# Kernel tuning notes

Measured on AMD Instinct MI355X. Metric: run time of the kernel, lower is better.

The kernel has to match this reference:

```python
import jax, jax.numpy as jnp
import numpy as np

D = 768       # GATv2 in/out feats (num_heads=1)
D_OUT = 384   # fc output
K = 51        # round(top_rate * L) = round(0.1 * 512)
EPS = 1e-5    # nn.LayerNorm default eps


def _layer_norm(x, g, b):
    mu = jnp.mean(x, axis=-1, keepdims=True)
    var = jnp.mean((x - mu) ** 2, axis=-1, keepdims=True)
    return (x - mu) / jnp.sqrt(var + EPS) * g + b


def setup_inputs() -> dict:
    key = jax.random.key(0)
    ks = jax.random.split(key, 12)
    B, L = 4, 512
    s = 0.02
    return {
        "hidden_state": jax.random.normal(ks[0], (B, L, D), jnp.float32),
        "attention": jax.random.uniform(ks[1], (B, L, L), jnp.float32),
        # GATv2Conv params (fc_src, fc_dst, attn vector, output bias)
        "W_src": jax.random.normal(ks[2], (D, D), jnp.float32) * s,
        "b_src": jnp.zeros((D,), jnp.float32),
        "W_dst": jax.random.normal(ks[3], (D, D), jnp.float32) * s,
        "b_dst": jnp.zeros((D,), jnp.float32),
        "attn_vec": jax.random.normal(ks[4], (D,), jnp.float32) * s,
        "gat_bias": jnp.zeros((D,), jnp.float32),
        # GlobalAttentionPooling gate_nn: Linear(768, 1)
        "gate_W": jax.random.normal(ks[5], (D, 1), jnp.float32) * s,
        "gate_b": jnp.zeros((1,), jnp.float32),
        # LayerNorm(768)
        "ln_g": jnp.ones((D,), jnp.float32),
        "ln_b": jnp.zeros((D,), jnp.float32),
        # fc: Linear(768, 384)
        "fc_W": jax.random.normal(ks[6], (D, D_OUT), jnp.float32) * s,
        "fc_b": jnp.zeros((D_OUT,), jnp.float32),
        # LayerNorm(384)
        "ln2_g": jnp.ones((D_OUT,), jnp.float32),
        "ln2_b": jnp.zeros((D_OUT,), jnp.float32),
        "mask": jnp.ones((B, L), jnp.int32),  # unused by the original forward
        "type": 0,                              # unused string/type flag
    }


def reference(hidden_state, attention, W_src, b_src, W_dst, b_dst, attn_vec,
              gat_bias, gate_W, gate_b, ln_g, ln_b, fc_W, fc_b, ln2_g, ln2_b,
              mask, type):
    B, L, _ = hidden_state.shape
    # --- topk sparsification: each node i keeps K source neighbors ---
    vals, idx = jax.lax.top_k(attention, K)          # [B, L, K]
    valid = vals > 0.0                                # edges kept by pos_sign filter

    # --- GATv2Conv (num_heads=1, residual=Identity since 768==768) ---
    feat_src = hidden_state @ W_src + b_src           # [B, L, D]
    feat_dst = hidden_state @ W_dst + b_dst           # [B, L, D]
    g = feat_src[jnp.arange(B)[:, None, None], idx]   # [B, L, K, D] gathered src feats
    e = jax.nn.leaky_relu(g + feat_dst[:, :, None, :], 0.2)
    scores = jnp.einsum("blkd,d->blk", e, attn_vec)   # [B, L, K]
    scores = jnp.where(valid, scores, -1e9)           # removed edges masked out
    a = jax.nn.softmax(scores, axis=-1)               # edge_softmax per dst node
    h = jnp.einsum("blk,blkd->bld", a, g)             # weighted scatter-sum
    h = h + hidden_state + gat_bias                   # residual (identity) + bias
    h = jax.nn.leaky_relu(h, 0.01)                    # nn.LeakyReLU activation

    # --- GlobalAttentionPooling: softmax(gate) weighted segment reduce ---
    gate = h @ gate_W + gate_b                        # [B, L, 1]
    p = jax.nn.softmax(gate, axis=1)
    pooled = jnp.sum(p * h, axis=1)                   # [B, D]

    # --- head: fc(dropout(ln(relu(out)))) then ln2 (dropout = eval identity) ---
    out = _layer_norm(jax.nn.relu(pooled), ln_g, ln_b)
    out = out @ fc_W + fc_b
    out = _layer_norm(out, ln2_g, ln2_b)
    return out
```

## Files before the change

kernel.cpp:

```cpp
#include <hip/hip_runtime.h>
#include <math.h>

#define D 768
#define DOUT 384
#define LSEQ 512
#define BATCH 4
#define KTOP 51
#define EPS 1e-5f

typedef unsigned short ushort_t;
typedef __bf16 bf16x8 __attribute__((ext_vector_type(8)));
typedef float f32x4 __attribute__((ext_vector_type(4)));

#define GLOAD16(gp, lp)                                                        \
    __builtin_amdgcn_global_load_lds(                                          \
        (const __attribute__((address_space(1))) unsigned int*)(gp),           \
        (__attribute__((address_space(3))) unsigned int*)(lp), 16, 0, 0)

__device__ __forceinline__ ushort_t f2bf(float f) {
    unsigned int u = __builtin_bit_cast(unsigned int, f);
    u = (u + 0x7FFFu + ((u >> 16) & 1u)) >> 16;
    return (ushort_t)u;
}

__global__ __launch_bounds__(256) void prep_kernel(const float* __restrict__ hidden,
                                                   ushort_t* __restrict__ Ah,
                                                   const float* __restrict__ W0,
                                                   const float* __restrict__ W1,
                                                   ushort_t* __restrict__ WT0,
                                                   ushort_t* __restrict__ WT1) {
    __shared__ float tile[32][33];
    const int bid = blockIdx.x;
    const int tid = threadIdx.x;
    if (bid < 1536) {
        const int i = (bid * 256 + tid) * 4;
        const float4 v = *(const float4*)(hidden + i);
        ushort4 o;
        o.x = f2bf(v.x); o.y = f2bf(v.y); o.z = f2bf(v.z); o.w = f2bf(v.w);
        *(ushort4*)(Ah + i) = o;
    } else {
        const int t = bid - 1536;
        const int zz = t / 576;
        const int rem = t - zz * 576;
        const int by = rem / 24, bx = rem - by * 24;
        const float* W = zz ? W1 : W0;
        ushort_t* WT = zz ? WT1 : WT0;
        const int kbase = by * 32;
        const int nbase = bx * 32;
        const int r = tid >> 3, c4 = (tid & 7) * 4;

        const float4 v = *(const float4*)(W + (size_t)(kbase + r) * D + nbase + c4);
        tile[r][c4 + 0] = v.x; tile[r][c4 + 1] = v.y;
        tile[r][c4 + 2] = v.z; tile[r][c4 + 3] = v.w;
        __syncthreads();
        ushort4 o;
        o.x = f2bf(tile[c4 + 0][r]); o.y = f2bf(tile[c4 + 1][r]);
        o.z = f2bf(tile[c4 + 2][r]); o.w = f2bf(tile[c4 + 3][r]);
        *(ushort4*)(WT + (size_t)(nbase + r) * D + kbase + c4) = o;
    }
}

__global__ __launch_bounds__(256) void feat_gemm_kernel(const ushort_t* __restrict__ Ah,
                                                        const ushort_t* __restrict__ WT0,
                                                        const float* __restrict__ b0,
                                                        ushort_t* __restrict__ Csrc_bf,
                                                        const ushort_t* __restrict__ WT1,
                                                        const float* __restrict__ b1,
                                                        float* __restrict__ Cdst) {
    const ushort_t* WT = blockIdx.z ? WT1 : WT0;
    const float* bias = blockIdx.z ? b1 : b0;

    __shared__ ushort_t As[64 * 32];
    __shared__ ushort_t Bs[64 * 32];

    const int tid = threadIdx.x;
    const int lane = tid & 63;
    const int wave = tid >> 6;
    const int quad = lane >> 4;
    const int m15 = lane & 15;
    const int qRow = (wave & 1) * 32;
    const int qCol = (wave >> 1) * 32;

    const int rowBase = blockIdx.y * 64;
    const int colBase = blockIdx.x * 64;

    const int e0 = tid * 8;
    const int r0 = e0 >> 5;
    const int c0 = e0 & 31;
    const ushort_t* Abase = Ah + (size_t)rowBase * D;
    const ushort_t* Bbase = WT + (size_t)colBase * D;

    f32x4 acc[2][2] = {};

    for (int kk = 0; kk < D; kk += 32) {
        __syncthreads();
        GLOAD16(Abase + (size_t)r0 * D + kk + c0, &As[e0]);
        GLOAD16(Bbase + (size_t)r0 * D + kk + c0, &Bs[e0]);
        __syncthreads();

        bf16x8 a[2], b[2];
#pragma unroll
        for (int i = 0; i < 2; ++i)
            a[i] = *(const bf16x8*)&As[(qRow + i * 16 + m15) * 32 + quad * 8];
#pragma unroll
        for (int j = 0; j < 2; ++j)
            b[j] = *(const bf16x8*)&Bs[(qCol + j * 16 + m15) * 32 + quad * 8];
#pragma unroll
        for (int i = 0; i < 2; ++i)
#pragma unroll
            for (int j = 0; j < 2; ++j)
                acc[i][j] = __builtin_amdgcn_mfma_f32_16x16x32_bf16(a[i], b[j], acc[i][j], 0, 0, 0);
    }

    if (blockIdx.z == 0) {
#pragma unroll
        for (int j = 0; j < 2; ++j) {
            const int col = colBase + qCol + j * 16 + m15;
            const float bv = bias[col];
#pragma unroll
            for (int i = 0; i < 2; ++i) {
                ushort_t* Cp = Csrc_bf + (size_t)(rowBase + qRow + i * 16 + quad * 4) * D + col;
#pragma unroll
                for (int r = 0; r < 4; ++r)
                    Cp[(size_t)r * D] = f2bf(acc[i][j][r] + bv);
            }
        }
    } else {
#pragma unroll
        for (int j = 0; j < 2; ++j) {
            const int col = colBase + qCol + j * 16 + m15;
            const float bv = bias[col];
#pragma unroll
            for (int i = 0; i < 2; ++i) {
                float* Cp = Cdst + (size_t)(rowBase + qRow + i * 16 + quad * 4) * D + col;
#pragma unroll
                for (int r = 0; r < 4; ++r)
                    Cp[(size_t)r * D] = acc[i][j][r] + bv;
            }
        }
    }
}

__global__ __launch_bounds__(256) void transpose_fsrc_kernel(const ushort_t* __restrict__ I,
                                                             ushort_t* __restrict__ O) {
    __shared__ ushort_t tile[32][33];
    const int b = blockIdx.z;
    const int cbase = blockIdx.x * 32;
    const int rbase = blockIdx.y * 32;
    const int tid = threadIdx.x;
    const int tr = tid >> 3, tc4 = (tid & 7) * 4;

    const ushort_t* Ib = I + (size_t)b * LSEQ * D;
    ushort_t* Ob = O + (size_t)b * D * LSEQ;

    const ushort4 v = *(const ushort4*)(Ib + (size_t)(rbase + tr) * D + cbase + tc4);
    tile[tr][tc4 + 0] = v.x; tile[tr][tc4 + 1] = v.y;
    tile[tr][tc4 + 2] = v.z; tile[tr][tc4 + 3] = v.w;
    __syncthreads();
    ushort4 o;
    o.x = tile[tc4 + 0][tr]; o.y = tile[tc4 + 1][tr];
    o.z = tile[tc4 + 2][tr]; o.w = tile[tc4 + 3][tr];
    *(ushort4*)(Ob + (size_t)(cbase + tr) * LSEQ + rbase + tc4) = o;
}

__global__ __launch_bounds__(256) void score_kernel(const float* __restrict__ attn,
                                                    const ushort_t* __restrict__ fsrc_bf,
                                                    const float* __restrict__ feat_dst,
                                                    const float* __restrict__ attn_vec,
                                                    const float* __restrict__ gate_b,
                                                    ushort_t* __restrict__ P,
                                                    float* __restrict__ gate) {
    const int row = blockIdx.x;
    const int b = row >> 9;
    const int tid = threadIdx.x;
    const int lane = tid & 63;
    const int wave = tid >> 6;

    __shared__ float vals[LSEQ];
    __shared__ float cval[320];
    __shared__ int   cidx[320];
    __shared__ int   nhi, outSlot;
    __shared__ float sc[KTOP];
    __shared__ int   kid[KTOP];
    __shared__ float kvv[KTOP];

    ((unsigned int*)(P + (size_t)row * LSEQ))[tid] = 0u;
    if (tid == 0) { gate[row] = gate_b[0]; nhi = 0; outSlot = 0; }

    const float* a = attn + (size_t)row * LSEQ;
    const float v0 = a[tid];
    const float v1 = a[tid + 256];
    vals[tid] = v0;
    vals[tid + 256] = v1;
    __syncthreads();

    if (v0 > 0.75f) {
        const int s = atomicAdd(&nhi, 1);
        if (s < 320) { cval[s] = v0; cidx[s] = tid; }
    }
    if (v1 > 0.75f) {
        const int s = atomicAdd(&nhi, 1);
        if (s < 320) { cval[s] = v1; cidx[s] = tid + 256; }
    }
    __syncthreads();

    const int n = nhi;
    if (n >= KTOP && n <= 320) {
        if (tid < n) {
            const float v = cval[tid];
            const int e = cidx[tid];
            int r = 0;
            for (int j = 0; j < n; ++j) {
                const float u = cval[j];
                r += (u > v) || (u == v && cidx[j] < e);
            }
            if (r < KTOP) {
                const int s = atomicAdd(&outSlot, 1);
                kid[s] = e; kvv[s] = v;
            }
        }
    } else {
#pragma unroll
        for (int e0 = 0; e0 < 2; ++e0) {
            const int e = tid + e0 * 256;
            const float v = vals[e];
            int r = 0;
            for (int j = 0; j < LSEQ; ++j) {
                const float u = vals[j];
                r += (u > v) || (u == v && j < e);
            }
            if (r < KTOP) {
                const int s = atomicAdd(&outSlot, 1);
                kid[s] = e; kvv[s] = v;
            }
        }
    }

    const float* fdp = feat_dst + (size_t)row * D;
    float fdr[16], avr[16];
    {
        const int d0 = lane * 8;
        const float4 f0 = *(const float4*)(fdp + d0);
        const float4 f1 = *(const float4*)(fdp + d0 + 4);
        const float4 a0 = *(const float4*)(attn_vec + d0);
        const float4 a1 = *(const float4*)(attn_vec + d0 + 4);
        fdr[0]=f0.x; fdr[1]=f0.y; fdr[2]=f0.z; fdr[3]=f0.w;
        fdr[4]=f1.x; fdr[5]=f1.y; fdr[6]=f1.z; fdr[7]=f1.w;
        avr[0]=a0.x; avr[1]=a0.y; avr[2]=a0.z; avr[3]=a0.w;
        avr[4]=a1.x; avr[5]=a1.y; avr[6]=a1.z; avr[7]=a1.w;
    }
    if (lane < 32) {
        const int d1 = (lane + 64) * 8;
        const float4 f0 = *(const float4*)(fdp + d1);
        const float4 f1 = *(const float4*)(fdp + d1 + 4);
        const float4 a0 = *(const float4*)(attn_vec + d1);
        const float4 a1 = *(const float4*)(attn_vec + d1 + 4);
        fdr[8]=f0.x; fdr[9]=f0.y; fdr[10]=f0.z; fdr[11]=f0.w;
        fdr[12]=f1.x; fdr[13]=f1.y; fdr[14]=f1.z; fdr[15]=f1.w;
        avr[8]=a0.x; avr[9]=a0.y; avr[10]=a0.z; avr[11]=a0.w;
        avr[12]=a1.x; avr[13]=a1.y; avr[14]=a1.z; avr[15]=a1.w;
    }
    __syncthreads();

    for (int k = wave; k < KTOP; k += 4) {
        const ushort_t* g = fsrc_bf + ((size_t)(b << 9) + kid[k]) * D;
        float s = 0.f;
        const bf16x8 g0 = *(const bf16x8*)(g + lane * 8);
#pragma unroll
        for (int jj = 0; jj < 8; ++jj) {
            float x = (float)g0[jj] + fdr[jj];
            x = x > 0.f ? x : 0.2f * x;
            s += x * avr[jj];
        }
        if (lane < 32) {
            const bf16x8 g1 = *(const bf16x8*)(g + (lane + 64) * 8);
#pragma unroll
            for (int jj = 0; jj < 8; ++jj) {
                float x = (float)g1[jj] + fdr[8 + jj];
                x = x > 0.f ? x : 0.2f * x;
                s += x * avr[8 + jj];
            }
        }
#pragma unroll
        for (int off = 32; off > 0; off >>= 1) s += __shfl_down(s, off);
        if (lane == 0) sc[k] = (kvv[k] > 0.f) ? s : -1e9f;
    }
    __syncthreads();

    if (wave == 0) {
        float s = (lane < KTOP) ? sc[lane] : -3.0e38f;
        float m = s;
#pragma unroll
        for (int off = 32; off > 0; off >>= 1) m = fmaxf(m, __shfl_xor(m, off));
        float e = (lane < KTOP) ? __expf(s - m) : 0.f;
        float sum = e;
#pragma unroll
        for (int off = 32; off > 0; off >>= 1) sum += __shfl_xor(sum, off);
        if (lane < KTOP) sc[lane] = e / sum;
    }
    __syncthreads();

    if (tid < KTOP)
        P[(size_t)row * LSEQ + kid[tid]] = f2bf(sc[tid]);
}

__global__ __launch_bounds__(256) void pgemm_kernel(const ushort_t* __restrict__ P,
                                                    const ushort_t* __restrict__ fsrcT,
                                                    const float* __restrict__ gat_bias,
                                                    const float* __restrict__ hidden,
                                                    const float* __restrict__ gate_W,
                                                    float* __restrict__ h,
                                                    float* __restrict__ gate) {
    const int bb = blockIdx.z;
    const ushort_t* Ab = P + (size_t)bb * LSEQ * LSEQ;
    const ushort_t* Bb = fsrcT + (size_t)bb * D * LSEQ;

    __shared__ ushort_t As[64 * 32];
    __shared__ ushort_t Bs[64 * 32];

    const int tid = threadIdx.x;
    const int lane = tid & 63;
    const int wave = tid >> 6;
    const int quad = lane >> 4;
    const int m15 = lane & 15;
    const int qRow = (wave & 1) * 32;
    const int qCol = (wave >> 1) * 32;

    const int rowBase = blockIdx.y * 64;
    const int colBase = blockIdx.x * 64;

    const int e0 = tid * 8;
    const int r0 = e0 >> 5;
    const int c0 = e0 & 31;
    const ushort_t* Abase = Ab + (size_t)rowBase * LSEQ;
    const ushort_t* Bbase = Bb + (size_t)colBase * LSEQ;

    f32x4 acc[2][2] = {};

    for (int kk = 0; kk < LSEQ; kk += 32) {
        __syncthreads();
        GLOAD16(Abase + (size_t)r0 * LSEQ + kk + c0, &As[e0]);
        GLOAD16(Bbase + (size_t)r0 * LSEQ + kk + c0, &Bs[e0]);
        __syncthreads();

        bf16x8 a[2], b[2];
#pragma unroll
        for (int i = 0; i < 2; ++i)
            a[i] = *(const bf16x8*)&As[(qRow + i * 16 + m15) * 32 + quad * 8];
#pragma unroll
        for (int j = 0; j < 2; ++j)
            b[j] = *(const bf16x8*)&Bs[(qCol + j * 16 + m15) * 32 + quad * 8];
#pragma unroll
        for (int i = 0; i < 2; ++i)
#pragma unroll
            for (int j = 0; j < 2; ++j)
                acc[i][j] = __builtin_amdgcn_mfma_f32_16x16x32_bf16(a[i], b[j], acc[i][j], 0, 0, 0);
    }

    const float* hidb = hidden + (size_t)bb * LSEQ * D;
    float* hb = h + (size_t)bb * LSEQ * D;
    float rp[2][4] = {};
#pragma unroll
    for (int j = 0; j < 2; ++j) {
        const int col = colBase + qCol + j * 16 + m15;
        const float bv = gat_bias[col];
        const float gw = gate_W[col];
#pragma unroll
        for (int i = 0; i < 2; ++i) {
            const int row0 = rowBase + qRow + i * 16 + quad * 4;
#pragma unroll
            for (int r = 0; r < 4; ++r) {
                float v = acc[i][j][r] + bv + hidb[(size_t)(row0 + r) * D + col];
                v = v > 0.f ? v : 0.01f * v;
                hb[(size_t)(row0 + r) * D + col] = v;
                rp[i][r] += v * gw;
            }
        }
    }
#pragma unroll
    for (int i = 0; i < 2; ++i)
#pragma unroll
        for (int r = 0; r < 4; ++r) {
            float p4 = rp[i][r];
            p4 += __shfl_xor(p4, 1);
            p4 += __shfl_xor(p4, 2);
            p4 += __shfl_xor(p4, 4);
            p4 += __shfl_xor(p4, 8);
            if (m15 == 0)
                atomicAdd(&gate[bb * LSEQ + rowBase + qRow + i * 16 + quad * 4 + r], p4);
        }
}

__global__ __launch_bounds__(256) void gatesm_kernel(const float* __restrict__ gate,
                                                     float* __restrict__ p,
                                                     float* __restrict__ pooled,
                                                     float* __restrict__ z) {
    const int b = blockIdx.x;
    const int tid = threadIdx.x;
    __shared__ float red[256];

    const float g0 = gate[b * LSEQ + tid];
    const float g1 = gate[b * LSEQ + tid + 256];
    red[tid] = fmaxf(g0, g1);
    __syncthreads();
    for (int s = 128; s > 0; s >>= 1) { if (tid < s) red[tid] = fmaxf(red[tid], red[tid + s]); __syncthreads(); }
    const float m = red[0];
    __syncthreads();
    const float e0 = __expf(g0 - m), e1 = __expf(g1 - m);
    red[tid] = e0 + e1;
    __syncthreads();
    for (int s = 128; s > 0; s >>= 1) { if (tid < s) red[tid] += red[tid + s]; __syncthreads(); }
    const float inv = 1.f / red[0];
    p[b * LSEQ + tid] = e0 * inv;
    p[b * LSEQ + tid + 256] = e1 * inv;

    for (int d = tid; d < D; d += 256) pooled[b * D + d] = 0.f;
    if (tid < 128) { z[b * DOUT + tid] = 0.f; z[b * DOUT + tid + 128] = 0.f; z[b * DOUT + tid + 256] = 0.f; }
}

__global__ __launch_bounds__(256) void pool_kernel(const float* __restrict__ h,
                                                   const float* __restrict__ p,
                                                   float* __restrict__ pooled) {
    const int b = blockIdx.z;
    const int lbase = blockIdx.y * 64;
    const int d = blockIdx.x * 256 + threadIdx.x;
    const int tid = threadIdx.x;

    __shared__ float ps[64];
    if (tid < 64) ps[tid] = p[b * LSEQ + lbase + tid];
    __syncthreads();

    const float* hb = h + ((size_t)(b * LSEQ + lbase)) * D + d;
    float acc = 0.f;
#pragma unroll 8
    for (int l = 0; l < 64; ++l) {
        acc += ps[l] * hb[(size_t)l * D];
    }
    atomicAdd(&pooled[b * D + d], acc);
}

__global__ __launch_bounds__(256) void ln1_kernel(const float* __restrict__ pooled,
                                                  const float* __restrict__ ln_g,
                                                  const float* __restrict__ ln_b,
                                                  float* __restrict__ y) {
    const int b = blockIdx.x;
    const int tid = threadIdx.x;
    __shared__ float red[256];

    float v[3];
#pragma unroll
    for (int i = 0; i < 3; ++i) v[i] = fmaxf(pooled[b * D + tid + i * 256], 0.f);

    red[tid] = v[0] + v[1] + v[2];
    __syncthreads();
    for (int s = 128; s > 0; s >>= 1) { if (tid < s) red[tid] += red[tid + s]; __syncthreads(); }
    const float mu = red[0] / (float)D;
    __syncthreads();
    float vs = 0.f;
#pragma unroll
    for (int i = 0; i < 3; ++i) { const float dd = v[i] - mu; vs += dd * dd; }
    red[tid] = vs;
    __syncthreads();
    for (int s = 128; s > 0; s >>= 1) { if (tid < s) red[tid] += red[tid + s]; __syncthreads(); }
    const float rstd = rsqrtf(red[0] / (float)D + EPS);
#pragma unroll
    for (int i = 0; i < 3; ++i) {
        const int d = tid + i * 256;
        y[b * D + d] = (v[i] - mu) * rstd * ln_g[d] + ln_b[d];
    }
}

__global__ __launch_bounds__(256) void fc_kernel(const float* __restrict__ y,
                                                 const float* __restrict__ fc_W,
                                                 float* __restrict__ z) {
    const int b = blockIdx.z;
    const int dbase = blockIdx.y * 256;
    const int jbase = blockIdx.x * 64;
    const int tid = threadIdx.x;
    const int jt = tid & 63;
    const int sub = tid >> 6;

    __shared__ float ys[256];
    __shared__ float part[4][64];
    ys[tid] = y[b * D + dbase + tid];
    __syncthreads();

    const float* W = fc_W + (size_t)(dbase + sub * 64) * DOUT + jbase + jt;
    const float* yy = ys + sub * 64;
    float acc = 0.f;
#pragma unroll 8
    for (int i = 0; i < 64; ++i) {
        acc += yy[i] * W[(size_t)i * DOUT];
    }
    part[sub][jt] = acc;
    __syncthreads();
    if (sub == 0) {
        const float tot = part[0][jt] + part[1][jt] + part[2][jt] + part[3][jt];
        atomicAdd(&z[b * DOUT + jbase + jt], tot);
    }
}

__global__ __launch_bounds__(384) void ln2_kernel(const float* __restrict__ z,
                                                  const float* __restrict__ fc_b,
                                                  const float* __restrict__ ln2_g,
                                                  const float* __restrict__ ln2_b,
                                                  float* __restrict__ out) {
    const int b = blockIdx.x;
    const int tid = threadIdx.x;
    const int lane = tid & 63;
    const int wave = tid >> 6;
    __shared__ float wred[6];

    const float v = z[b * DOUT + tid] + fc_b[tid];

    float s = v;
#pragma unroll
    for (int off = 32; off > 0; off >>= 1) s += __shfl_xor(s, off);
    if (lane == 0) wred[wave] = s;
    __syncthreads();
    float mu = 0.f;
#pragma unroll
    for (int w = 0; w < 6; ++w) mu += wred[w];
    mu /= (float)DOUT;
    __syncthreads();

    const float dd = v - mu;
    float s2 = dd * dd;
#pragma unroll
    for (int off = 32; off > 0; off >>= 1) s2 += __shfl_xor(s2, off);
    if (lane == 0) wred[wave] = s2;
    __syncthreads();
    float var = 0.f;
#pragma unroll
    for (int w = 0; w < 6; ++w) var += wred[w];
    const float rstd = rsqrtf(var / (float)DOUT + EPS);

    out[b * DOUT + tid] = dd * rstd * ln2_g[tid] + ln2_b[tid];
}

extern "C" void kernel_launch(void* const* d_in, const int* in_sizes, int n_in,
                              void* d_out, int out_size, void* d_ws, size_t ws_size,
                              hipStream_t stream) {
    const float* hidden   = (const float*)d_in[0];
    const float* attention= (const float*)d_in[1];
    const float* W_src    = (const float*)d_in[2];
    const float* b_src    = (const float*)d_in[3];
    const float* W_dst    = (const float*)d_in[4];
    const float* b_dst    = (const float*)d_in[5];
    const float* attn_vec = (const float*)d_in[6];
    const float* gat_bias = (const float*)d_in[7];
    const float* gate_W   = (const float*)d_in[8];
    const float* gate_b   = (const float*)d_in[9];
    const float* ln_g     = (const float*)d_in[10];
    const float* ln_b     = (const float*)d_in[11];
    const float* fc_W     = (const float*)d_in[12];
    const float* fc_b     = (const float*)d_in[13];
    const float* ln2_g    = (const float*)d_in[14];
    const float* ln2_b    = (const float*)d_in[15];
    float* out = (float*)d_out;

    const int M = BATCH * LSEQ;
    float* feat_dst = (float*)d_ws;
    float* h        = feat_dst + (size_t)M * D;
    float* gate     = h + (size_t)M * D;
    float* p        = gate + M;
    float* pooled   = p + BATCH * LSEQ;
    float* y        = pooled + BATCH * D;
    float* z        = y + BATCH * D;
    ushort_t* Ah    = (ushort_t*)(z + BATCH * DOUT);
    ushort_t* WT0   = Ah + (size_t)M * D;
    ushort_t* WT1   = WT0 + (size_t)D * D;
    ushort_t* fsrcb = WT1 + (size_t)D * D;
    ushort_t* fsrcT = fsrcb + (size_t)M * D;
    ushort_t* P     = fsrcT + (size_t)M * D;

    hipLaunchKernelGGL(prep_kernel, dim3(2688), dim3(256), 0, stream,
                       hidden, Ah, W_src, W_dst, WT0, WT1);
    hipLaunchKernelGGL(feat_gemm_kernel, dim3(D / 64, M / 64, 2), dim3(256), 0, stream,
                       Ah, WT0, b_src, fsrcb, WT1, b_dst, feat_dst);
    hipLaunchKernelGGL(transpose_fsrc_kernel, dim3(D / 32, LSEQ / 32, BATCH), dim3(256), 0, stream,
                       fsrcb, fsrcT);
    hipLaunchKernelGGL(score_kernel, dim3(M), dim3(256), 0, stream,
                       attention, fsrcb, feat_dst, attn_vec, gate_b, P, gate);
    hipLaunchKernelGGL(pgemm_kernel, dim3(D / 64, LSEQ / 64, BATCH), dim3(256), 0, stream,
                       P, fsrcT, gat_bias, hidden, gate_W, h, gate);
    hipLaunchKernelGGL(gatesm_kernel, dim3(BATCH), dim3(256), 0, stream,
                       gate, p, pooled, z);
    hipLaunchKernelGGL(pool_kernel, dim3(D / 256, LSEQ / 64, BATCH), dim3(256), 0, stream,
                       h, p, pooled);
    hipLaunchKernelGGL(ln1_kernel, dim3(BATCH), dim3(256), 0, stream,
                       pooled, ln_g, ln_b, y);
    hipLaunchKernelGGL(fc_kernel, dim3(DOUT / 64, D / 256, BATCH), dim3(256), 0, stream,
                       y, fc_W, z);
    hipLaunchKernelGGL(ln2_kernel, dim3(BATCH), dim3(384), 0, stream,
                       z, fc_b, ln2_g, ln2_b, out);
}
```

Measured before the change: 180.5 us.

## Fuse gate softmax into pooling and LayerNorm into fc; store h as bf16

```diff
diff --git a/kernel.cpp b/kernel.cpp
--- a/kernel.cpp
+++ b/kernel.cpp
@@ -23,12 +23,19 @@
     return (ushort_t)u;
 }
 
+__device__ __forceinline__ float bf2f(ushort_t u) {
+    unsigned int v = ((unsigned int)u) << 16;
+    return __builtin_bit_cast(float, v);
+}
+
 __global__ __launch_bounds__(256) void prep_kernel(const float* __restrict__ hidden,
                                                    ushort_t* __restrict__ Ah,
                                                    const float* __restrict__ W0,
                                                    const float* __restrict__ W1,
                                                    ushort_t* __restrict__ WT0,
-                                                   ushort_t* __restrict__ WT1) {
+                                                   ushort_t* __restrict__ WT1,
+                                                   float* __restrict__ pooled,
+                                                   float* __restrict__ z) {
     __shared__ float tile[32][33];
     const int bid = blockIdx.x;
     const int tid = threadIdx.x;
@@ -38,7 +45,7 @@
         ushort4 o;
         o.x = f2bf(v.x); o.y = f2bf(v.y); o.z = f2bf(v.z); o.w = f2bf(v.w);
         *(ushort4*)(Ah + i) = o;
-    } else {
+    } else if (bid < 2688) {
         const int t = bid - 1536;
         const int zz = t / 576;
         const int rem = t - zz * 576;
@@ -57,6 +64,9 @@
         o.x = f2bf(tile[c4 + 0][r]); o.y = f2bf(tile[c4 + 1][r]);
         o.z = f2bf(tile[c4 + 2][r]); o.w = f2bf(tile[c4 + 3][r]);
         *(ushort4*)(WT + (size_t)(nbase + r) * D + kbase + c4) = o;
+    } else {
+        for (int i = tid; i < BATCH * D; i += 256) pooled[i] = 0.f;
+        for (int i = tid; i < BATCH * DOUT; i += 256) z[i] = 0.f;
     }
 }
 
@@ -309,7 +319,7 @@
                                                     const float* __restrict__ gat_bias,
                                                     const float* __restrict__ hidden,
                                                     const float* __restrict__ gate_W,
-                                                    float* __restrict__ h,
+                                                    ushort_t* __restrict__ h,
                                                     float* __restrict__ gate) {
     const int bb = blockIdx.z;
     const ushort_t* Ab = P + (size_t)bb * LSEQ * LSEQ;
@@ -358,7 +368,7 @@
     }
 
     const float* hidb = hidden + (size_t)bb * LSEQ * D;
-    float* hb = h + (size_t)bb * LSEQ * D;
+    ushort_t* hb = h + (size_t)bb * LSEQ * D;
     float rp[2][4] = {};
 #pragma unroll
     for (int j = 0; j < 2; ++j) {
@@ -372,7 +382,7 @@
             for (int r = 0; r < 4; ++r) {
                 float v = acc[i][j][r] + bv + hidb[(size_t)(row0 + r) * D + col];
                 v = v > 0.f ? v : 0.01f * v;
-                hb[(size_t)(row0 + r) * D + col] = v;
+                hb[(size_t)(row0 + r) * D + col] = f2bf(v);
                 rp[i][r] += v * gw;
             }
         }
@@ -391,98 +401,76 @@
         }
 }
 
-__global__ __launch_bounds__(256) void gatesm_kernel(const float* __restrict__ gate,
-                                                     float* __restrict__ p,
-                                                     float* __restrict__ pooled,
-                                                     float* __restrict__ z) {
-    const int b = blockIdx.x;
-    const int tid = threadIdx.x;
-    __shared__ float red[256];
-
-    const float g0 = gate[b * LSEQ + tid];
-    const float g1 = gate[b * LSEQ + tid + 256];
-    red[tid] = fmaxf(g0, g1);
-    __syncthreads();
-    for (int s = 128; s > 0; s >>= 1) { if (tid < s) red[tid] = fmaxf(red[tid], red[tid + s]); __syncthreads(); }
-    const float m = red[0];
-    __syncthreads();
-    const float e0 = __expf(g0 - m), e1 = __expf(g1 - m);
-    red[tid] = e0 + e1;
-    __syncthreads();
-    for (int s = 128; s > 0; s >>= 1) { if (tid < s) red[tid] += red[tid + s]; __syncthreads(); }
-    const float inv = 1.f / red[0];
-    p[b * LSEQ + tid] = e0 * inv;
-    p[b * LSEQ + tid + 256] = e1 * inv;
-
-    for (int d = tid; d < D; d += 256) pooled[b * D + d] = 0.f;
-    if (tid < 128) { z[b * DOUT + tid] = 0.f; z[b * DOUT + tid + 128] = 0.f; z[b * DOUT + tid + 256] = 0.f; }
-}
-
-__global__ __launch_bounds__(256) void pool_kernel(const float* __restrict__ h,
-                                                   const float* __restrict__ p,
+__global__ __launch_bounds__(256) void pool_kernel(const ushort_t* __restrict__ h,
+                                                   const float* __restrict__ gate,
                                                    float* __restrict__ pooled) {
     const int b = blockIdx.z;
     const int lbase = blockIdx.y * 64;
     const int d = blockIdx.x * 256 + threadIdx.x;
     const int tid = threadIdx.x;
 
+    __shared__ float red[256];
     __shared__ float ps[64];
-    if (tid < 64) ps[tid] = p[b * LSEQ + lbase + tid];
-    __syncthreads();
-
-    const float* hb = h + ((size_t)(b * LSEQ + lbase)) * D + d;
+
+    const float g0 = gate[b * LSEQ + tid];
+    const float g1 = gate[b * LSEQ + tid + 256];
+    red[tid] = fmaxf(g0, g1);
+    __syncthreads();
+    for (int s = 128; s > 0; s >>= 1) { if (tid < s) red[tid] = fmaxf(red[tid], red[tid + s]); __syncthreads(); }
+    const float m = red[0];
+    __syncthreads();
+    red[tid] = __expf(g0 - m) + __expf(g1 - m);
+    __syncthreads();
+    for (int s = 128; s > 0; s >>= 1) { if (tid < s) red[tid] += red[tid + s]; __syncthreads(); }
+    const float inv = 1.f / red[0];
+    if (tid < 64) ps[tid] = __expf(gate[b * LSEQ + lbase + tid] - m) * inv;
+    __syncthreads();
+
+    const ushort_t* hb = h + ((size_t)(b * LSEQ + lbase)) * D + d;
     float acc = 0.f;
 #pragma unroll 8
     for (int l = 0; l < 64; ++l) {
-        acc += ps[l] * hb[(size_t)l * D];
+        acc += ps[l] * bf2f(hb[(size_t)l * D]);
     }
     atomicAdd(&pooled[b * D + d], acc);
 }
 
-__global__ __launch_bounds__(256) void ln1_kernel(const float* __restrict__ pooled,
-                                                  const float* __restrict__ ln_g,
-                                                  const float* __restrict__ ln_b,
-                                                  float* __restrict__ y) {
-    const int b = blockIdx.x;
-    const int tid = threadIdx.x;
-    __shared__ float red[256];
-
-    float v[3];
-#pragma unroll
-    for (int i = 0; i < 3; ++i) v[i] = fmaxf(pooled[b * D + tid + i * 256], 0.f);
-
-    red[tid] = v[0] + v[1] + v[2];
-    __syncthreads();
-    for (int s = 128; s > 0; s >>= 1) { if (tid < s) red[tid] += red[tid + s]; __syncthreads(); }
-    const float mu = red[0] / (float)D;
-    __syncthreads();
-    float vs = 0.f;
-#pragma unroll
-    for (int i = 0; i < 3; ++i) { const float dd = v[i] - mu; vs += dd * dd; }
-    red[tid] = vs;
-    __syncthreads();
-    for (int s = 128; s > 0; s >>= 1) { if (tid < s) red[tid] += red[tid + s]; __syncthreads(); }
-    const float rstd = rsqrtf(red[0] / (float)D + EPS);
-#pragma unroll
-    for (int i = 0; i < 3; ++i) {
-        const int d = tid + i * 256;
-        y[b * D + d] = (v[i] - mu) * rstd * ln_g[d] + ln_b[d];
-    }
-}
-
-__global__ __launch_bounds__(256) void fc_kernel(const float* __restrict__ y,
+__global__ __launch_bounds__(256) void fc_kernel(const float* __restrict__ pooled,
+                                                 const float* __restrict__ ln_g,
+                                                 const float* __restrict__ ln_b,
                                                  const float* __restrict__ fc_W,
                                                  float* __restrict__ z) {
     const int b = blockIdx.z;
-    const int dbase = blockIdx.y * 256;
+    const int by = blockIdx.y;
+    const int dbase = by * 256;
     const int jbase = blockIdx.x * 64;
     const int tid = threadIdx.x;
     const int jt = tid & 63;
     const int sub = tid >> 6;
 
+    __shared__ float red[256];
     __shared__ float ys[256];
     __shared__ float part[4][64];
-    ys[tid] = y[b * D + dbase + tid];
+
+    float v[3];
+#pragma unroll
+    for (int i = 0; i < 3; ++i) v[i] = fmaxf(pooled[b * D + tid + i * 256], 0.f);
+
+    red[tid] = v[0] + v[1] + v[2];
+    __syncthreads();
+    for (int s = 128; s > 0; s >>= 1) { if (tid < s) red[tid] += red[tid + s]; __syncthreads(); }
+    const float mu = red[0] / (float)D;
+    __syncthreads();
+    float vs = 0.f;
+#pragma unroll
+    for (int i = 0; i < 3; ++i) { const float dd = v[i] - mu; vs += dd * dd; }
+    red[tid] = vs;
+    __syncthreads();
+    for (int s = 128; s > 0; s >>= 1) { if (tid < s) red[tid] += red[tid + s]; __syncthreads(); }
+    const float rstd = rsqrtf(red[0] / (float)D + EPS);
+
+    const float vb = (by == 0) ? v[0] : (by == 1 ? v[1] : v[2]);
+    ys[tid] = (vb - mu) * rstd * ln_g[dbase + tid] + ln_b[dbase + tid];
     __syncthreads();
 
     const float* W = fc_W + (size_t)(dbase + sub * 64) * DOUT + jbase + jt;
@@ -561,21 +549,19 @@
 
     const int M = BATCH * LSEQ;
     float* feat_dst = (float*)d_ws;
-    float* h        = feat_dst + (size_t)M * D;
-    float* gate     = h + (size_t)M * D;
-    float* p        = gate + M;
-    float* pooled   = p + BATCH * LSEQ;
-    float* y        = pooled + BATCH * D;
-    float* z        = y + BATCH * D;
+    float* gate     = feat_dst + (size_t)M * D;
+    float* pooled   = gate + M;
+    float* z        = pooled + BATCH * D;
     ushort_t* Ah    = (ushort_t*)(z + BATCH * DOUT);
     ushort_t* WT0   = Ah + (size_t)M * D;
     ushort_t* WT1   = WT0 + (size_t)D * D;
     ushort_t* fsrcb = WT1 + (size_t)D * D;
     ushort_t* fsrcT = fsrcb + (size_t)M * D;
     ushort_t* P     = fsrcT + (size_t)M * D;
-
-    hipLaunchKernelGGL(prep_kernel, dim3(2688), dim3(256), 0, stream,
-                       hidden, Ah, W_src, W_dst, WT0, WT1);
+    ushort_t* h     = P + (size_t)M * LSEQ;
+
+    hipLaunchKernelGGL(prep_kernel, dim3(2689), dim3(256), 0, stream,
+                       hidden, Ah, W_src, W_dst, WT0, WT1, pooled, z);
     hipLaunchKernelGGL(feat_gemm_kernel, dim3(D / 64, M / 64, 2), dim3(256), 0, stream,
                        Ah, WT0, b_src, fsrcb, WT1, b_dst, feat_dst);
     hipLaunchKernelGGL(transpose_fsrc_kernel, dim3(D / 32, LSEQ / 32, BATCH), dim3(256), 0, stream,
@@ -584,14 +570,10 @@
                        attention, fsrcb, feat_dst, attn_vec, gate_b, P, gate);
     hipLaunchKernelGGL(pgemm_kernel, dim3(D / 64, LSEQ / 64, BATCH), dim3(256), 0, stream,
                        P, fsrcT, gat_bias, hidden, gate_W, h, gate);
-    hipLaunchKernelGGL(gatesm_kernel, dim3(BATCH), dim3(256), 0, stream,
-                       gate, p, pooled, z);
     hipLaunchKernelGGL(pool_kernel, dim3(D / 256, LSEQ / 64, BATCH), dim3(256), 0, stream,
-                       h, p, pooled);
-    hipLaunchKernelGGL(ln1_kernel, dim3(BATCH), dim3(256), 0, stream,
-                       pooled, ln_g, ln_b, y);
+                       h, gate, pooled);
     hipLaunchKernelGGL(fc_kernel, dim3(DOUT / 64, D / 256, BATCH), dim3(256), 0, stream,
-                       y, fc_W, z);
+                       pooled, ln_g, ln_b, fc_W, z);
     hipLaunchKernelGGL(ln2_kernel, dim3(BATCH), dim3(384), 0, stream,
                        z, fc_b, ln2_g, ln2_b, out);
 }
```

After: 177.3 us (median of 2 runs). Within noise of the previous version (-1.8%).
